# Optimization experiments

Measured on AMD Instinct MI355X. Metric: run time of the kernel, lower is better.

Reference implementation:

```python
import jax, jax.numpy as jnp
import numpy as np

# EXP-HYDRO concrete realization of HydrologyModel.
# Parameter order matches _parameter_bounds key order; bounds per standard EXP-HYDRO.
PARAM_BOUNDS = [
    ("f",    0.0,  0.1),
    ("Smax", 100.0, 1500.0),
    ("Qmax", 10.0, 50.0),
    ("Df",   0.0,  5.0),
    ("Tmax", 0.0,  3.0),
    ("Tmin", -3.0, 0.0),
]
NEARZERO = 1e-6
T_STEPS = 1024
N_BASINS = 8192
N_PARAMS = len(PARAM_BOUNDS)


def _denormalize(static_params_norm):
    # sigmoid activation then affine map to bounds; returns dict name -> [B]
    act = jax.nn.sigmoid(static_params_norm)  # [B, P]
    return {name: lo + (hi - lo) * act[:, i]
            for i, (name, lo, hi) in enumerate(PARAM_BOUNDS)}


def _run_core(prcp, temp, pet, params, nearzero=NEARZERO):
    # prcp/temp/pet: [T, B]; params: dict of [B]
    f, Smax, Qmax = params["f"], params["Smax"], params["Qmax"]
    Df, Tmax, Tmin = params["Df"], params["Tmax"], params["Tmin"]

    def step(states, forc_t):
        snowpack, soilwater = states
        prcp_t, temp_t, pet_t = forc_t
        # hydroflux formulas (elementwise over basins)
        snowfall = jnp.where(temp_t < Tmin, prcp_t, 0.0)
        rainfall = prcp_t - snowfall
        melt = jnp.minimum(snowpack, Df * jnp.maximum(temp_t - Tmax, 0.0))
        evap = pet_t * jnp.minimum(soilwater / Smax, 1.0)
        baseflow = Qmax * jnp.exp(-f * jnp.maximum(Smax - soilwater, 0.0))
        surfaceflow = jnp.maximum(soilwater - Smax, 0.0)
        # stateflux formulas (state changes)
        d_snow = snowfall - melt
        d_soil = rainfall + melt - evap - baseflow - surfaceflow
        # state update with clamp(min=nearzero)
        new_snow = jnp.maximum(snowpack + d_snow, nearzero)
        new_soil = jnp.maximum(soilwater + d_soil, nearzero)
        out = jnp.stack([snowfall, rainfall, melt, evap,
                         baseflow, surfaceflow, d_snow, d_soil])  # [8, B]
        return (new_snow, new_soil), out

    B = prcp.shape[1]
    init = (jnp.zeros((B,), prcp.dtype), jnp.zeros((B,), prcp.dtype))
    _, outs = jax.lax.scan(step, init, (prcp, temp, pet))
    return outs  # [T, 8, B]


def setup_inputs() -> dict:
    key = jax.random.key(0)
    k1, k2, k3, k4 = jax.random.split(key, 4)
    prcp = jax.random.uniform(k1, (T_STEPS, N_BASINS), jnp.float32) * 10.0  # mm/day
    temp = jax.random.normal(k2, (T_STEPS, N_BASINS), jnp.float32) * 5.0    # deg C
    pet = jax.random.uniform(k3, (T_STEPS, N_BASINS), jnp.float32) * 5.0    # mm/day
    static_params_norm = jax.random.normal(k4, (N_BASINS, N_PARAMS), jnp.float32)
    return {"prcp": prcp, "temp": temp, "pet": pet,
            "static_params_norm": static_params_norm}


def reference(prcp, temp, pet, static_params_norm):
    params = _denormalize(static_params_norm)
    return _run_core(prcp, temp, pet, params)  # [T, 8, B]
```

## Files before the change

kernel.cpp:

```cpp
#include <hip/hip_runtime.h>
#include <stdint.h>

#define NB 8192
#define TSTEPS 1024
#define OUT_TSTRIDE (8 * NB)
#define TILE 32
#define LDS_F 6144


__device__ __forceinline__ float sigmoidf_(float x) {
    return 1.0f / (1.0f + __expf(-x));
}

__device__ __forceinline__ void async16(const float* g, float* l) {
    __builtin_amdgcn_global_load_lds(
        (const __attribute__((address_space(1))) void*)g,
        (__attribute__((address_space(3))) void*)l, 16, 0, 0);
}

struct Params {
    float f, Smax, Qmax, Df, Tmax, Tmin, rSmax, nf;
};

__device__ __forceinline__ Params load_params(const float* __restrict__ spn,
                                              int basin) {
    const float* p6 = spn + (size_t)basin * 6;
    Params p;
    p.f     = 0.1f * sigmoidf_(p6[0]);
    p.Smax  = 100.0f + 1400.0f * sigmoidf_(p6[1]);
    p.Qmax  = 10.0f + 40.0f * sigmoidf_(p6[2]);
    p.Df    = 5.0f * sigmoidf_(p6[3]);
    p.Tmax  = 3.0f * sigmoidf_(p6[4]);
    p.Tmin  = -3.0f + 3.0f * sigmoidf_(p6[5]);
    p.rSmax = 1.0f / p.Smax;
    p.nf    = -p.f;
    return p;
}

struct Flux {
    float snowfall, rainfall, melt, evap, baseflow, surfaceflow, d_snow, d_soil;
};

__device__ __forceinline__ Flux hydro_step(const Params& p, float& snow,
                                           float& soil, float P, float Tm,
                                           float Pe) {
    Flux o;
    o.snowfall    = (Tm < p.Tmin) ? P : 0.0f;
    o.rainfall    = P - o.snowfall;
    o.melt        = fminf(snow, p.Df * fmaxf(Tm - p.Tmax, 0.0f));
    o.evap        = Pe * fminf(soil * p.rSmax, 1.0f);
    o.baseflow    = p.Qmax * __expf(p.nf * fmaxf(p.Smax - soil, 0.0f));
    o.surfaceflow = fmaxf(soil - p.Smax, 0.0f);
    o.d_snow      = o.snowfall - o.melt;
    o.d_soil = (((o.rainfall + o.melt) - o.evap) - o.baseflow) - o.surfaceflow;
    snow = fmaxf(snow + o.d_snow, 1e-6f);
    soil = fmaxf(soil + o.d_soil, 1e-6f);
    return o;
}

__device__ __forceinline__ void fill64(const float* __restrict__ prcp,
                                       const float* __restrict__ temp,
                                       const float* __restrict__ pet,
                                       float* lds, int t0, int lane,
                                       int gbase) {
#pragma unroll
    for (int k = 0; k < 24; ++k) {
        const float* src = (k < 8) ? prcp : ((k < 16) ? temp : pet);
        int row = ((k & 7) << 2) + (lane >> 4);
        int t   = t0 + row;
        t       = (t > TSTEPS - 1) ? (TSTEPS - 1) : t;
        const float* g = src + (size_t)t * NB + gbase + ((lane & 15) << 2);
        float* l       = lds + (k << 8) + (lane << 2);
        async16(g, l);
    }
}

template <int SEGLEN>
__global__ void __launch_bounds__(64)
hydro_phase1(const float* __restrict__ prcp, const float* __restrict__ temp,
             const float* __restrict__ pet, const float* __restrict__ spn,
             float* __restrict__ ckpt) {
    __shared__ float lds[2][LDS_F];
    const int lane  = threadIdx.x;
    const int g     = blockIdx.x;
    const int gbase = g * 64;
    const int basin = gbase + lane;

    const Params prm = load_params(spn, basin);
    float snow = 0.0f, soil = 0.0f;

    fill64(prcp, temp, pet, lds[0], 0, lane, gbase);
    __syncthreads();

    for (int tile = 0; tile < TSTEPS / TILE; ++tile) {
        const int cur = tile & 1;
        fill64(prcp, temp, pet, lds[cur ^ 1], (tile + 1) * TILE, lane, gbase);

        const float* lp = lds[cur];
#pragma unroll 16
        for (int i = 0; i < TILE; ++i) {
            const int t = tile * TILE + i;
            if ((t & (SEGLEN - 1)) == 0) {
                const int s = t / SEGLEN;
                ckpt[(size_t)(2 * s) * NB + basin]     = snow;
                ckpt[(size_t)(2 * s + 1) * NB + basin] = soil;
            }
            const float P  = lp[i * 64 + lane];
            const float Tm = lp[2048 + i * 64 + lane];
            const float Pe = lp[4096 + i * 64 + lane];
            (void)hydro_step(prm, snow, soil, P, Tm, Pe);
        }
        __syncthreads();
    }
}

template <int SEGLEN>
__global__ void __launch_bounds__(256, 4)
hydro_phase2(const float* __restrict__ prcp, const float* __restrict__ temp,
             const float* __restrict__ pet, const float* __restrict__ spn,
             const float* __restrict__ ckpt, float* __restrict__ out) {
    const int tid   = threadIdx.x;
    const int lane  = tid & 63;
    const int wid   = (blockIdx.x << 2) + (tid >> 6);
    const int g     = wid & 127;
    const int s     = wid >> 7;
    const int basin = g * 64 + lane;

    const Params prm = load_params(spn, basin);

    float snow, soil;
    if (SEGLEN == 1024) {
        snow = 0.0f;
        soil = 0.0f;
    } else {
        snow = ckpt[(size_t)(2 * s) * NB + basin];
        soil = ckpt[(size_t)(2 * s + 1) * NB + basin];
    }

    const int t0 = s * SEGLEN;
#pragma unroll 8
    for (int i = 0; i < SEGLEN; ++i) {
        const int t     = t0 + i;
        const size_t fo = (size_t)t * NB + basin;
        const float P   = prcp[fo];
        const float Tm  = temp[fo];
        const float Pe  = pet[fo];

        const Flux fl = hydro_step(prm, snow, soil, P, Tm, Pe);

        float* o = out + (size_t)t * OUT_TSTRIDE + basin;
        o[0 * NB] = fl.snowfall;
        o[1 * NB] = fl.rainfall;
        o[2 * NB] = fl.melt;
        o[3 * NB] = fl.evap;
        o[4 * NB] = fl.baseflow;
        o[5 * NB] = fl.surfaceflow;
        o[6 * NB] = fl.d_snow;
        o[7 * NB] = fl.d_soil;
    }
}

extern "C" void kernel_launch(void* const* d_in, const int* in_sizes, int n_in,
                              void* d_out, int out_size, void* d_ws,
                              size_t ws_size, hipStream_t stream) {
    const float* prcp = (const float*)d_in[0];
    const float* temp = (const float*)d_in[1];
    const float* pet  = (const float*)d_in[2];
    const float* spn  = (const float*)d_in[3];
    float* out        = (float*)d_out;
    float* ckpt       = (float*)d_ws;

    const size_t need32  = (size_t)(TSTEPS / 32) * 2 * NB * sizeof(float);
    const size_t need128 = (size_t)(TSTEPS / 128) * 2 * NB * sizeof(float);

    if (ws_size >= need32) {
        hydro_phase1<32><<<dim3(128), dim3(64), 0, stream>>>(prcp, temp, pet,
                                                             spn, ckpt);
        hydro_phase2<32><<<dim3(1024), dim3(256), 0, stream>>>(
            prcp, temp, pet, spn, ckpt, out);
    } else if (ws_size >= need128) {
        hydro_phase1<128><<<dim3(128), dim3(64), 0, stream>>>(prcp, temp, pet,
                                                              spn, ckpt);
        hydro_phase2<128><<<dim3(256), dim3(256), 0, stream>>>(
            prcp, temp, pet, spn, ckpt, out);
    } else {
        hydro_phase2<1024><<<dim3(32), dim3(256), 0, stream>>>(
            prcp, temp, pet, spn, nullptr, out);
    }
}
```

Measured before the change: 400.2 us.

## Fuse scan and output phases into one producer-consumer kernel with LDS checkpoints

Replaces the two-kernel scheme with a single kernel of 128 blocks. In each block, one wavefront runs the serial state scan over LDS-staged forcing tiles and writes per-tile states into LDS. Two consumer wavefronts replay each 32-step tile in 16-step halves from those states and write the eight flux outputs to global memory. This removes the global checkpoint round-trip, the second global read of the forcings and a kernel launch, and overlaps the serial scan with the output stores. The cost is that only 128 blocks run, so output write bandwidth rests on 256 consumer waves, and a four-deep LDS ring with a barrier every round.

```diff
diff --git a/kernel.cpp b/kernel.cpp
--- a/kernel.cpp
+++ b/kernel.cpp
@@ -5,7 +5,10 @@
 #define TSTEPS 1024
 #define OUT_TSTRIDE (8 * NB)
 #define TILE 32
-#define LDS_F 6144
+#define NSEG (TSTEPS / TILE)
+#define NBUF 4
+#define TILE_F (3 * TILE * 64)
+#define HALF 16
 
 
 __device__ __forceinline__ float sigmoidf_(float x) {
@@ -75,88 +78,81 @@
     }
 }
 
-template <int SEGLEN>
-__global__ void __launch_bounds__(64)
-hydro_phase1(const float* __restrict__ prcp, const float* __restrict__ temp,
-             const float* __restrict__ pet, const float* __restrict__ spn,
-             float* __restrict__ ckpt) {
-    __shared__ float lds[2][LDS_F];
-    const int lane  = threadIdx.x;
+extern "C" __global__ void __launch_bounds__(192, 1)
+hydro_fused(const float* __restrict__ prcp, const float* __restrict__ temp,
+            const float* __restrict__ pet, const float* __restrict__ spn,
+            float* __restrict__ out) {
+    __shared__ float fbuf[NBUF][TILE_F];
+    __shared__ float ckpt[4][2][64];
+
+    const int tid   = threadIdx.x;
+    const int lane  = tid & 63;
+    const int w     = tid >> 6;
     const int g     = blockIdx.x;
     const int gbase = g * 64;
     const int basin = gbase + lane;
 
     const Params prm = load_params(spn, basin);
-    float snow = 0.0f, soil = 0.0f;
 
-    fill64(prcp, temp, pet, lds[0], 0, lane, gbase);
+    float psnow = 0.0f, psoil = 0.0f;
+    float csnow = 0.0f, csoil = 0.0f;
+
+    if (w == 0) fill64(prcp, temp, pet, fbuf[0], 0, lane, gbase);
     __syncthreads();
 
-    for (int tile = 0; tile < TSTEPS / TILE; ++tile) {
-        const int cur = tile & 1;
-        fill64(prcp, temp, pet, lds[cur ^ 1], (tile + 1) * TILE, lane, gbase);
+    for (int r = 0; r < NSEG + 2; ++r) {
+        if (w == 0) {
+            if (r < NSEG) {
+                ckpt[r & 3][0][lane] = psnow;
+                ckpt[r & 3][1][lane] = psoil;
+                if (r + 1 < NSEG)
+                    fill64(prcp, temp, pet, fbuf[(r + 1) & 3],
+                           (r + 1) * TILE, lane, gbase);
+                const float* lp = fbuf[r & 3];
+#pragma unroll 8
+                for (int i = 0; i < TILE; ++i) {
+                    const float P  = lp[i * 64 + lane];
+                    const float Tm = lp[2048 + i * 64 + lane];
+                    const float Pe = lp[4096 + i * 64 + lane];
+                    (void)hydro_step(prm, psnow, psoil, P, Tm, Pe);
+                }
+            }
+        } else {
+            const int c = w - 1;
+            int s, phase;
+            if (((r - 1) & 1) == c) { s = r - 1; phase = 0; }
+            else                    { s = r - 2; phase = 1; }
+            if (s >= 0 && s < NSEG) {
+                if (phase == 0) {
+                    csnow = ckpt[s & 3][0][lane];
+                    csoil = ckpt[s & 3][1][lane];
+                }
+                const float* lp = fbuf[s & 3];
+                float* o = out +
+                           (size_t)(s * TILE + phase * HALF) * OUT_TSTRIDE +
+                           gbase + lane;
+#pragma unroll 4
+                for (int i = 0; i < HALF; ++i) {
+                    const int row  = phase * HALF + i;
+                    const float P  = lp[row * 64 + lane];
+                    const float Tm = lp[2048 + row * 64 + lane];
+                    const float Pe = lp[4096 + row * 64 + lane];
 
-        const float* lp = lds[cur];
-#pragma unroll 16
-        for (int i = 0; i < TILE; ++i) {
-            const int t = tile * TILE + i;
-            if ((t & (SEGLEN - 1)) == 0) {
-                const int s = t / SEGLEN;
-                ckpt[(size_t)(2 * s) * NB + basin]     = snow;
-                ckpt[(size_t)(2 * s + 1) * NB + basin] = soil;
+                    const Flux fl = hydro_step(prm, csnow, csoil, P, Tm, Pe);
+
+                    o[0 * NB] = fl.snowfall;
+                    o[1 * NB] = fl.rainfall;
+                    o[2 * NB] = fl.melt;
+                    o[3 * NB] = fl.evap;
+                    o[4 * NB] = fl.baseflow;
+                    o[5 * NB] = fl.surfaceflow;
+                    o[6 * NB] = fl.d_snow;
+                    o[7 * NB] = fl.d_soil;
+                    o += OUT_TSTRIDE;
+                }
             }
-            const float P  = lp[i * 64 + lane];
-            const float Tm = lp[2048 + i * 64 + lane];
-            const float Pe = lp[4096 + i * 64 + lane];
-            (void)hydro_step(prm, snow, soil, P, Tm, Pe);
         }
         __syncthreads();
-    }
-}
-
-template <int SEGLEN>
-__global__ void __launch_bounds__(256, 4)
-hydro_phase2(const float* __restrict__ prcp, const float* __restrict__ temp,
-             const float* __restrict__ pet, const float* __restrict__ spn,
-             const float* __restrict__ ckpt, float* __restrict__ out) {
-    const int tid   = threadIdx.x;
-    const int lane  = tid & 63;
-    const int wid   = (blockIdx.x << 2) + (tid >> 6);
-    const int g     = wid & 127;
-    const int s     = wid >> 7;
-    const int basin = g * 64 + lane;
-
-    const Params prm = load_params(spn, basin);
-
-    float snow, soil;
-    if (SEGLEN == 1024) {
-        snow = 0.0f;
-        soil = 0.0f;
-    } else {
-        snow = ckpt[(size_t)(2 * s) * NB + basin];
-        soil = ckpt[(size_t)(2 * s + 1) * NB + basin];
-    }
-
-    const int t0 = s * SEGLEN;
-#pragma unroll 8
-    for (int i = 0; i < SEGLEN; ++i) {
-        const int t     = t0 + i;
-        const size_t fo = (size_t)t * NB + basin;
-        const float P   = prcp[fo];
-        const float Tm  = temp[fo];
-        const float Pe  = pet[fo];
-
-        const Flux fl = hydro_step(prm, snow, soil, P, Tm, Pe);
-
-        float* o = out + (size_t)t * OUT_TSTRIDE + basin;
-        o[0 * NB] = fl.snowfall;
-        o[1 * NB] = fl.rainfall;
-        o[2 * NB] = fl.melt;
-        o[3 * NB] = fl.evap;
-        o[4 * NB] = fl.baseflow;
-        o[5 * NB] = fl.surfaceflow;
-        o[6 * NB] = fl.d_snow;
-        o[7 * NB] = fl.d_soil;
     }
 }
 
@@ -168,23 +164,7 @@
     const float* pet  = (const float*)d_in[2];
     const float* spn  = (const float*)d_in[3];
     float* out        = (float*)d_out;
-    float* ckpt       = (float*)d_ws;
 
-    const size_t need32  = (size_t)(TSTEPS / 32) * 2 * NB * sizeof(float);
-    const size_t need128 = (size_t)(TSTEPS / 128) * 2 * NB * sizeof(float);
-
-    if (ws_size >= need32) {
-        hydro_phase1<32><<<dim3(128), dim3(64), 0, stream>>>(prcp, temp, pet,
-                                                             spn, ckpt);
-        hydro_phase2<32><<<dim3(1024), dim3(256), 0, stream>>>(
-            prcp, temp, pet, spn, ckpt, out);
-    } else if (ws_size >= need128) {
-        hydro_phase1<128><<<dim3(128), dim3(64), 0, stream>>>(prcp, temp, pet,
-                                                              spn, ckpt);
-        hydro_phase2<128><<<dim3(256), dim3(256), 0, stream>>>(
-            prcp, temp, pet, spn, ckpt, out);
-    } else {
-        hydro_phase2<1024><<<dim3(32), dim3(256), 0, stream>>>(
-            prcp, temp, pet, spn, nullptr, out);
-    }
+    hydro_fused<<<dim3(128), dim3(192), 0, stream>>>(prcp, temp, pet, spn,
+                                                     out);
 }
```

After: 385.0 us. 1.04x faster.
